# Kernel tuning notes

Hardware: AMD Instinct MI355X
Metric: run time of the kernel (lower is better)

## Reference

```python
import jax, jax.numpy as jnp
import numpy as np

N = 20000      # nodes
E = 640000     # edges
FIN = 128
FQK = 128
FV = 128
H = 8
FH = FQK // H   # 16
FHV = FV // H   # 16
FTOT = 2 * FQK + FV


def setup_inputs() -> dict:
    key = jax.random.key(0)
    kx, kw, ks, kd, kb = jax.random.split(key, 5)
    x = jax.random.normal(kx, (N, FIN), dtype=jnp.float32)
    # nn.Linear(Fin, Ftot, bias=False): weight [Ftot, Fin]
    W = jax.random.normal(kw, (FTOT, FIN), dtype=jnp.float32) / np.sqrt(FIN)
    # src must be sorted (scatter ops assume grouped-by-src, size src[-1]+1)
    src = jnp.sort(jax.random.randint(ks, (E,), 0, N, dtype=jnp.int64))
    src = src.at[-1].set(N - 1)  # ensure full output size N
    dest = jax.random.randint(kd, (E,), 0, N, dtype=jnp.int64)
    ei = jnp.stack([src, dest])
    batch = jnp.sort(jax.random.randint(kb, (N,), 0, 16, dtype=jnp.int64))
    return {"x": x, "W": W, "batch": batch, "ei": ei}


def reference(x, W, batch, ei):
    src, dest = ei[0], ei[1]
    scaling = float(FH) ** (-0.5)
    proj = x @ W.T                                  # [N, Ftot]
    q, k, v = jnp.split(proj, [FQK, 2 * FQK], axis=-1)
    q = (q * scaling).reshape(-1, H, FH)            # [N, H, Fh]
    k = k.reshape(-1, H, FH)
    v = v.reshape(-1, H, FHV)
    qs, ks, vs = q[src], k[dest], v[dest]           # [E, H, Fh] gathers
    aw = jnp.einsum('ehf,ehf->eh', qs, ks)          # per-edge dot products
    # scatter_softmax: global (not per-segment) max subtraction, as in source
    xm = aw.max(axis=0)                              # [H]
    exp = jnp.exp(aw - xm) + 1e-8                    # [E, H]
    expsum = jax.ops.segment_sum(exp, src, num_segments=N)[src]
    attn = exp / expsum                              # [E, H]
    out = jax.ops.segment_sum(attn[:, :, None] * vs, src, num_segments=N)
    return out.reshape(-1, H * FHV)                  # [N, Fv]
```

## Files before the change

### kernel.cpp

```cpp
#include <hip/hip_runtime.h>

constexpr int FIN = 128;

constexpr float XM0 = 8.0f;

typedef __attribute__((ext_vector_type(8))) short bf8x;
typedef __attribute__((ext_vector_type(4))) float f4x;
typedef _Float16 h2 __attribute__((ext_vector_type(2)));

__device__ inline unsigned short f2bf(float v) {
  unsigned int u = __float_as_uint(v);
  unsigned int r = u + 0x7FFFu + ((u >> 16) & 1u);
  return (unsigned short)(r >> 16);
}
__device__ inline float bf2f(unsigned short s) {
  return __uint_as_float(((unsigned int)s) << 16);
}
__device__ inline unsigned short f2h(float v) {
  _Float16 h = (_Float16)v;
  return __builtin_bit_cast(unsigned short, h);
}
__device__ inline h2 bch2(float f) { return __builtin_bit_cast(h2, f); }
__device__ inline float bcf(h2 h) { return __builtin_bit_cast(float, h); }

__device__ inline float dot2acc(h2 a, h2 b, float c) {
#if __has_builtin(__builtin_amdgcn_fdot2)
  return __builtin_amdgcn_fdot2(a, b, c, false);
#else
  return c + (float)a[0] * (float)b[0] + (float)a[1] * (float)b[1];
#endif
}

__global__ __launch_bounds__(256, 2) void proj_kernel(
    const float* __restrict__ x, const float* __restrict__ W,
    unsigned short* __restrict__ qg, unsigned short* __restrict__ kvg, int N,
    const int* __restrict__ src, const int* __restrict__ dest,
    unsigned short* __restrict__ dest16, int* __restrict__ row_ptr, int E) {
  __shared__ unsigned short xhi[128][72], xlo[128][72];
  __shared__ unsigned short whi[128][72], wlo[128][72];

  const int tid = threadIdx.x;
  const int r0 = blockIdx.y * 128;
  const int c0 = blockIdx.x * 128;

  {
    const int gid = (blockIdx.y * gridDim.x + blockIdx.x) * 256 + tid;
    const int tot = gridDim.x * gridDim.y * 256;
    for (int i = gid; i < E; i += tot) dest16[i] = (unsigned short)dest[i];
    if (gid <= N) {
      int lo = 0, hi = E;
      while (lo < hi) {
        int mid = (lo + hi) >> 1;
        if (src[mid] < gid) lo = mid + 1; else hi = mid;
      }
      row_ptr[gid] = lo;
    }
  }

  const int lane = tid & 63;
  const int w = tid >> 6;
  const int mbase = (w >> 1) * 64;
  const int nbase = (w & 1) * 64;
  const int lr = lane & 15;
  const int q4 = lane >> 4;

  f4x acc[4][4];
#pragma unroll
  for (int mt = 0; mt < 4; ++mt)
#pragma unroll
    for (int nt = 0; nt < 4; ++nt)
#pragma unroll
      for (int k = 0; k < 4; ++k) acc[mt][nt][k] = 0.f;

  for (int p = 0; p < 2; ++p) {
    if (p) __syncthreads();
#pragma unroll
    for (int pass = 0; pass < 8; ++pass) {
      const int idx = tid + pass * 256;
      const int kq = idx & 15, r = idx >> 4;
      float4 xv = make_float4(0.f, 0.f, 0.f, 0.f);
      if (r0 + r < N) xv = *(const float4*)(x + (size_t)(r0 + r) * FIN + p * 64 + kq * 4);
      const float4 wv = *(const float4*)(W + (size_t)(c0 + r) * FIN + p * 64 + kq * 4);
      const float xa[4] = {xv.x, xv.y, xv.z, xv.w};
      const float wa[4] = {wv.x, wv.y, wv.z, wv.w};
      unsigned short xh[4], xl[4], wh[4], wl[4];
#pragma unroll
      for (int i = 0; i < 4; ++i) {
        xh[i] = f2bf(xa[i]); xl[i] = f2bf(xa[i] - bf2f(xh[i]));
        wh[i] = f2bf(wa[i]); wl[i] = f2bf(wa[i] - bf2f(wh[i]));
      }
      *(ushort4*)&xhi[r][kq * 4] = make_ushort4(xh[0], xh[1], xh[2], xh[3]);
      *(ushort4*)&xlo[r][kq * 4] = make_ushort4(xl[0], xl[1], xl[2], xl[3]);
      *(ushort4*)&whi[r][kq * 4] = make_ushort4(wh[0], wh[1], wh[2], wh[3]);
      *(ushort4*)&wlo[r][kq * 4] = make_ushort4(wl[0], wl[1], wl[2], wl[3]);
    }
    __syncthreads();

#pragma unroll
    for (int kit = 0; kit < 2; ++kit) {
      const int ko = kit * 32 + q4 * 8;
      bf8x ah[4], al[4], bh[4], bl[4];
#pragma unroll
      for (int i2 = 0; i2 < 4; ++i2) {
        ah[i2] = *(const bf8x*)&xhi[mbase + i2 * 16 + lr][ko];
        al[i2] = *(const bf8x*)&xlo[mbase + i2 * 16 + lr][ko];
        bh[i2] = *(const bf8x*)&whi[nbase + i2 * 16 + lr][ko];
        bl[i2] = *(const bf8x*)&wlo[nbase + i2 * 16 + lr][ko];
      }
#pragma unroll
      for (int mt = 0; mt < 4; ++mt)
#pragma unroll
        for (int nt = 0; nt < 4; ++nt) {
          acc[mt][nt] = __builtin_amdgcn_mfma_f32_16x16x32_bf16(ah[mt], bh[nt], acc[mt][nt], 0, 0, 0);
          acc[mt][nt] = __builtin_amdgcn_mfma_f32_16x16x32_bf16(ah[mt], bl[nt], acc[mt][nt], 0, 0, 0);
          acc[mt][nt] = __builtin_amdgcn_mfma_f32_16x16x32_bf16(al[mt], bh[nt], acc[mt][nt], 0, 0, 0);
        }
    }
  }

#pragma unroll
  for (int mt = 0; mt < 4; ++mt)
#pragma unroll
    for (int nt = 0; nt < 4; ++nt)
#pragma unroll
      for (int rr = 0; rr < 4; ++rr) {
        const int row = r0 + mbase + mt * 16 + q4 * 4 + rr;
        if (row < N) {
          const int c = c0 + nbase + nt * 16 + lr;
          const float v = acc[mt][nt][rr];
          if (c < 128) {
            const int head = c >> 4, g = head >> 2, hg = head & 3;
            const int seg = hg * 2 + ((c >> 3) & 1), feat = c & 7;
            qg[((size_t)g * N + row) * 64 + seg * 8 + feat] = f2h(v * 0.25f);
          } else if (c < 256) {
            const int cc = c - 128;
            const int head = cc >> 4, g = head >> 2, hg = head & 3;
            const int seg = hg * 2 + ((cc >> 3) & 1), feat = cc & 7;
            kvg[((size_t)g * N + row) * 128 + seg * 8 + feat] = f2h(v);
          } else {
            const int cc = c - 256;
            const int head = cc >> 4, g = head >> 2, hg = head & 3;
            const int seg = hg * 2 + ((cc >> 3) & 1), feat = cc & 7;
            kvg[((size_t)g * N + row) * 128 + 64 + seg * 8 + feat] = f2h(v);
          }
        }
      }
}

__global__ __launch_bounds__(512, 8) void attn_kernel(
    const unsigned short* __restrict__ qg_, const unsigned short* __restrict__ kvg_,
    const unsigned short* __restrict__ dest16, const int* __restrict__ row_ptr,
    float* __restrict__ out, int N) {
  const _Float16* qg = (const _Float16*)qg_;
  const _Float16* kvg = (const _Float16*)kvg_;

  const int lane = threadIdx.x & 63;
  const int wid = __builtin_amdgcn_readfirstlane(threadIdx.x >> 6);
  const int g = blockIdx.x & 1;
  const int n = (blockIdx.x >> 1) * 8 + wid;
  if (n >= N) return;

  const int seg = lane & 7;
  const int slot = lane >> 3;

  const int e0 = row_ptr[n], e1 = row_ptr[n + 1];

  h2 q2[4];
  {
    const float4 qv = *(const float4*)(qg + ((size_t)g * N + n) * 64 + seg * 8);
    q2[0] = bch2(qv.x); q2[1] = bch2(qv.y); q2[2] = bch2(qv.z); q2[3] = bch2(qv.w);
  }

  const _Float16* kvb = kvg + (size_t)g * N * 128;
  h2 acc4[4] = {h2{0, 0}, h2{0, 0}, h2{0, 0}, h2{0, 0}};
  float es = 0.f;

  for (int cb = e0; cb < e1; cb += 64) {
    const int ee = cb + lane;
    const int dv = dest16[(ee < e1) ? ee : (e1 - 1)];

    const int rem = e1 - cb;
    const int nch = (rem < 64) ? ((rem + 7) >> 3) : 8;

    auto ldkv = [&](int j, float4& kk, float4& vv) {
      const int sl = j * 8 + slot;
      const int d = __shfl(dv, sl);
      const _Float16* kp = kvb + (size_t)d * 128 + seg * 8;
      kk = *(const float4*)kp;
      vv = *(const float4*)(kp + 64);
    };

    auto comp = [&](int j, const float4& kk, const float4& vv) {
      float p = 0.f;
      p = dot2acc(q2[0], bch2(kk.x), p);
      p = dot2acc(q2[1], bch2(kk.y), p);
      p = dot2acc(q2[2], bch2(kk.z), p);
      p = dot2acc(q2[3], bch2(kk.w), p);
      const float s = p + __shfl_xor(p, 1);
      const int e = cb + j * 8 + slot;
      const float a = (e < e1) ? (__expf(s - XM0) + 1e-8f) : 0.f;
      es += a;
      const _Float16 a1 = (_Float16)a;
      const h2 av = {a1, a1};
      acc4[0] = __builtin_elementwise_fma(av, bch2(vv.x), acc4[0]);
      acc4[1] = __builtin_elementwise_fma(av, bch2(vv.y), acc4[1]);
      acc4[2] = __builtin_elementwise_fma(av, bch2(vv.z), acc4[2]);
      acc4[3] = __builtin_elementwise_fma(av, bch2(vv.w), acc4[3]);
    };

    float4 kkA, vvA, kkB, vvB;
    ldkv(0, kkA, vvA);
    ldkv(1, kkB, vvB);

    for (int j = 0; j < nch; j += 2) {
      float4 kkA2, vvA2, kkB2, vvB2;
      const bool pf = (j + 2 < nch);
      if (pf) { ldkv(j + 2, kkA2, vvA2); ldkv(j + 3, kkB2, vvB2); }
      comp(j, kkA, vvA);
      comp(j + 1, kkB, vvB);
      if (pf) { kkA = kkA2; vvA = vvA2; kkB = kkB2; vvB = vvB2; }
    }
  }

#pragma unroll
  for (int st = 8; st <= 32; st <<= 1) {
#pragma unroll
    for (int j = 0; j < 4; ++j) {
      const h2 o = bch2(__shfl_xor(bcf(acc4[j]), st));
      acc4[j] = acc4[j] + o;
    }
    es += __shfl_xor(es, st);
  }

  if (slot == 0) {
    const float inv = (e1 > e0) ? (1.0f / es) : 0.f;
    const int head = g * 4 + (seg >> 1);
    const int half = seg & 1;
    float o[8];
#pragma unroll
    for (int j = 0; j < 4; ++j) {
      o[2 * j] = (float)acc4[j][0] * inv;
      o[2 * j + 1] = (float)acc4[j][1] * inv;
    }
    float* op = out + (size_t)n * 128 + head * 16 + half * 8;
    *(float4*)op = make_float4(o[0], o[1], o[2], o[3]);
    *(float4*)(op + 4) = make_float4(o[4], o[5], o[6], o[7]);
  }
}

extern "C" void kernel_launch(void* const* d_in, const int* in_sizes, int n_in,
                              void* d_out, int out_size, void* d_ws, size_t ws_size,
                              hipStream_t stream) {
  const float* x = (const float*)d_in[0];
  const float* W = (const float*)d_in[1];
  const int* ei = (const int*)d_in[3];

  const int N = in_sizes[0] / FIN;
  const int E = in_sizes[3] / 2;
  const int* src = ei;
  const int* dst = ei + E;
  float* out = (float*)d_out;

  char* ws = (char*)d_ws;
  unsigned short* qg = (unsigned short*)ws;
  size_t off = (size_t)2 * N * 64 * sizeof(unsigned short);
  unsigned short* kvg = (unsigned short*)(ws + off);
  off += (size_t)2 * N * 128 * sizeof(unsigned short);
  unsigned short* dest16 = (unsigned short*)(ws + off);
  off += ((size_t)E * sizeof(unsigned short) + 15) & ~15ull;
  int* row_ptr = (int*)(ws + off);

  dim3 pgrid(3, (N + 127) / 128);
  proj_kernel<<<pgrid, 256, 0, stream>>>(x, W, qg, kvg, N, src, dst, dest16, row_ptr, E);
  attn_kernel<<<5000, 512, 0, stream>>>(qg, kvg, dest16, row_ptr, out, N);
}
```

Measured before the change: 117.2 us.

## Split heads into four groups of two to shrink per-group KV gather rows

The Q/K/V scratch layout goes from two groups of four heads to four groups of two heads. Each attention wave now handles 16 edges per step with 4 lanes per edge, and the launch doubles to 10000 blocks. The aim is a smaller per-group KV working set (64 halves per node per group) that fits the cache better during random dest gathers. In exchange, the dest indices and row pointers are reread once per group, four times in total. Nontemporal loads and stores are also added for q, dest and the output.

```diff
diff --git a/kernel.cpp b/kernel.cpp
--- a/kernel.cpp
+++ b/kernel.cpp
@@ -6,6 +6,7 @@
 
 typedef __attribute__((ext_vector_type(8))) short bf8x;
 typedef __attribute__((ext_vector_type(4))) float f4x;
+typedef float f4v __attribute__((ext_vector_type(4)));
 typedef _Float16 h2 __attribute__((ext_vector_type(2)));
 
 __device__ inline unsigned short f2bf(float v) {
@@ -129,19 +130,19 @@
           const int c = c0 + nbase + nt * 16 + lr;
           const float v = acc[mt][nt][rr];
           if (c < 128) {
-            const int head = c >> 4, g = head >> 2, hg = head & 3;
+            const int head = c >> 4, g = head >> 1, hg = head & 1;
             const int seg = hg * 2 + ((c >> 3) & 1), feat = c & 7;
-            qg[((size_t)g * N + row) * 64 + seg * 8 + feat] = f2h(v * 0.25f);
+            qg[((size_t)g * N + row) * 32 + seg * 8 + feat] = f2h(v * 0.25f);
           } else if (c < 256) {
             const int cc = c - 128;
-            const int head = cc >> 4, g = head >> 2, hg = head & 3;
+            const int head = cc >> 4, g = head >> 1, hg = head & 1;
             const int seg = hg * 2 + ((cc >> 3) & 1), feat = cc & 7;
-            kvg[((size_t)g * N + row) * 128 + seg * 8 + feat] = f2h(v);
+            kvg[((size_t)g * N + row) * 64 + seg * 8 + feat] = f2h(v);
           } else {
             const int cc = c - 256;
-            const int head = cc >> 4, g = head >> 2, hg = head & 3;
+            const int head = cc >> 4, g = head >> 1, hg = head & 1;
             const int seg = hg * 2 + ((cc >> 3) & 1), feat = cc & 7;
-            kvg[((size_t)g * N + row) * 128 + 64 + seg * 8 + feat] = f2h(v);
+            kvg[((size_t)g * N + row) * 64 + 32 + seg * 8 + feat] = f2h(v);
           }
         }
       }
@@ -156,64 +157,65 @@
 
   const int lane = threadIdx.x & 63;
   const int wid = __builtin_amdgcn_readfirstlane(threadIdx.x >> 6);
-  const int g = blockIdx.x & 1;
-  const int n = (blockIdx.x >> 1) * 8 + wid;
+  const int g = blockIdx.x & 3;
+  const int n = (blockIdx.x >> 2) * 8 + wid;
   if (n >= N) return;
 
-  const int seg = lane & 7;
-  const int slot = lane >> 3;
+  const int seg = lane & 3;
+  const int slot = lane >> 2;
 
   const int e0 = row_ptr[n], e1 = row_ptr[n + 1];
 
   h2 q2[4];
   {
-    const float4 qv = *(const float4*)(qg + ((size_t)g * N + n) * 64 + seg * 8);
-    q2[0] = bch2(qv.x); q2[1] = bch2(qv.y); q2[2] = bch2(qv.z); q2[3] = bch2(qv.w);
-  }
-
-  const _Float16* kvb = kvg + (size_t)g * N * 128;
+    const f4v qv = __builtin_nontemporal_load(
+        (const f4v*)(qg + ((size_t)g * N + n) * 32 + seg * 8));
+    q2[0] = bch2(qv[0]); q2[1] = bch2(qv[1]); q2[2] = bch2(qv[2]); q2[3] = bch2(qv[3]);
+  }
+
+  const _Float16* kvb = kvg + (size_t)g * N * 64;
   h2 acc4[4] = {h2{0, 0}, h2{0, 0}, h2{0, 0}, h2{0, 0}};
   float es = 0.f;
 
   for (int cb = e0; cb < e1; cb += 64) {
     const int ee = cb + lane;
-    const int dv = dest16[(ee < e1) ? ee : (e1 - 1)];
+    const int dv = __builtin_nontemporal_load(dest16 + ((ee < e1) ? ee : (e1 - 1)));
 
     const int rem = e1 - cb;
-    const int nch = (rem < 64) ? ((rem + 7) >> 3) : 8;
-
-    auto ldkv = [&](int j, float4& kk, float4& vv) {
-      const int sl = j * 8 + slot;
+    const int nch = (rem < 64) ? ((rem + 15) >> 4) : 4;
+
+    auto ldkv = [&](int j, f4v& kk, f4v& vv) {
+      const int sl = j * 16 + slot;
       const int d = __shfl(dv, sl);
-      const _Float16* kp = kvb + (size_t)d * 128 + seg * 8;
-      kk = *(const float4*)kp;
-      vv = *(const float4*)(kp + 64);
+      const _Float16* kp = kvb + (size_t)d * 64 + seg * 8;
+      kk = *(const f4v*)kp;
+      vv = *(const f4v*)(kp + 32);
     };
 
-    auto comp = [&](int j, const float4& kk, const float4& vv) {
+    auto comp = [&](int j, const f4v& kk, const f4v& vv) {
       float p = 0.f;
-      p = dot2acc(q2[0], bch2(kk.x), p);
-      p = dot2acc(q2[1], bch2(kk.y), p);
-      p = dot2acc(q2[2], bch2(kk.z), p);
-      p = dot2acc(q2[3], bch2(kk.w), p);
+      p = dot2acc(q2[0], bch2(kk[0]), p);
+      p = dot2acc(q2[1], bch2(kk[1]), p);
+      p = dot2acc(q2[2], bch2(kk[2]), p);
+      p = dot2acc(q2[3], bch2(kk[3]), p);
       const float s = p + __shfl_xor(p, 1);
-      const int e = cb + j * 8 + slot;
+      const int e = cb + j * 16 + slot;
       const float a = (e < e1) ? (__expf(s - XM0) + 1e-8f) : 0.f;
       es += a;
       const _Float16 a1 = (_Float16)a;
       const h2 av = {a1, a1};
-      acc4[0] = __builtin_elementwise_fma(av, bch2(vv.x), acc4[0]);
-      acc4[1] = __builtin_elementwise_fma(av, bch2(vv.y), acc4[1]);
-      acc4[2] = __builtin_elementwise_fma(av, bch2(vv.z), acc4[2]);
-      acc4[3] = __builtin_elementwise_fma(av, bch2(vv.w), acc4[3]);
+      acc4[0] = __builtin_elementwise_fma(av, bch2(vv[0]), acc4[0]);
+      acc4[1] = __builtin_elementwise_fma(av, bch2(vv[1]), acc4[1]);
+      acc4[2] = __builtin_elementwise_fma(av, bch2(vv[2]), acc4[2]);
+      acc4[3] = __builtin_elementwise_fma(av, bch2(vv[3]), acc4[3]);
     };
 
-    float4 kkA, vvA, kkB, vvB;
+    f4v kkA, vvA, kkB, vvB;
     ldkv(0, kkA, vvA);
     ldkv(1, kkB, vvB);
 
     for (int j = 0; j < nch; j += 2) {
-      float4 kkA2, vvA2, kkB2, vvB2;
+      f4v kkA2, vvA2, kkB2, vvB2;
       const bool pf = (j + 2 < nch);
       if (pf) { ldkv(j + 2, kkA2, vvA2); ldkv(j + 3, kkB2, vvB2); }
       comp(j, kkA, vvA);
@@ -223,7 +225,7 @@
   }
 
 #pragma unroll
-  for (int st = 8; st <= 32; st <<= 1) {
+  for (int st = 4; st <= 32; st <<= 1) {
 #pragma unroll
     for (int j = 0; j < 4; ++j) {
       const h2 o = bch2(__shfl_xor(bcf(acc4[j]), st));
@@ -234,17 +236,19 @@
 
   if (slot == 0) {
     const float inv = (e1 > e0) ? (1.0f / es) : 0.f;
-    const int head = g * 4 + (seg >> 1);
+    const int head = g * 2 + (seg >> 1);
     const int half = seg & 1;
-    float o[8];
-#pragma unroll
-    for (int j = 0; j < 4; ++j) {
-      o[2 * j] = (float)acc4[j][0] * inv;
-      o[2 * j + 1] = (float)acc4[j][1] * inv;
+    f4v o0, o1;
+#pragma unroll
+    for (int j = 0; j < 2; ++j) {
+      o0[2 * j] = (float)acc4[j][0] * inv;
+      o0[2 * j + 1] = (float)acc4[j][1] * inv;
+      o1[2 * j] = (float)acc4[j + 2][0] * inv;
+      o1[2 * j + 1] = (float)acc4[j + 2][1] * inv;
     }
     float* op = out + (size_t)n * 128 + head * 16 + half * 8;
-    *(float4*)op = make_float4(o[0], o[1], o[2], o[3]);
-    *(float4*)(op + 4) = make_float4(o[4], o[5], o[6], o[7]);
+    __builtin_nontemporal_store(o0, (f4v*)op);
+    __builtin_nontemporal_store(o1, (f4v*)(op + 4));
   }
 }
 
@@ -263,14 +267,14 @@
 
   char* ws = (char*)d_ws;
   unsigned short* qg = (unsigned short*)ws;
-  size_t off = (size_t)2 * N * 64 * sizeof(unsigned short);
+  size_t off = (size_t)4 * N * 32 * sizeof(unsigned short);
   unsigned short* kvg = (unsigned short*)(ws + off);
-  off += (size_t)2 * N * 128 * sizeof(unsigned short);
+  off += (size_t)4 * N * 64 * sizeof(unsigned short);
   unsigned short* dest16 = (unsigned short*)(ws + off);
   off += ((size_t)E * sizeof(unsigned short) + 15) & ~15ull;
   int* row_ptr = (int*)(ws + off);
 
   dim3 pgrid(3, (N + 127) / 128);
   proj_kernel<<<pgrid, 256, 0, stream>>>(x, W, qg, kvg, N, src, dst, dest16, row_ptr, E);
-  attn_kernel<<<5000, 512, 0, stream>>>(qg, kvg, dest16, row_ptr, out, N);
-}
+  attn_kernel<<<10000, 512, 0, stream>>>(qg, kvg, dest16, row_ptr, out, N);
+}
```

Result: slower. 129.6 us (+10.6%).
